# Kernel tuning notes

Hardware: AMD Instinct MI355X
Metric: run time of the kernel (lower is better)

Reference implementation:

```python
import jax, jax.numpy as jnp
import numpy as np
from jax import lax

DIM = 64
HEADS = 4
B, Q, V = 8, 128, 128


def _modrelu(z, b):
    m = jnp.abs(z)
    return z * (jax.nn.relu(m + b) / (m + 1e-5))


def _eunn_unitary(h, th1, ph1, th2, ph2, om):
    # tunable-style EUNN, capacity 2: even-pair rotations, odd-pair rotations, diagonal phase
    d = h.shape[-1]
    # layer 1: pairs (0,1),(2,3),...
    hp = h.reshape(*h.shape[:-1], d // 2, 2)
    a, b = hp[..., 0], hp[..., 1]
    c1, s1, e1 = jnp.cos(th1), jnp.sin(th1), jnp.exp(1j * ph1)
    h = jnp.stack([e1 * (c1 * a - s1 * b), s1 * a + c1 * b], -1).reshape(h.shape)
    # layer 2: pairs (1,2),(3,4),...,(d-3,d-2); endpoints pass through
    mid = h[..., 1:d - 1].reshape(*h.shape[:-1], d // 2 - 1, 2)
    a, b = mid[..., 0], mid[..., 1]
    c2, s2, e2 = jnp.cos(th2), jnp.sin(th2), jnp.exp(1j * ph2)
    mid2 = jnp.stack([e2 * (c2 * a - s2 * b), s2 * a + c2 * b], -1).reshape(*h.shape[:-1], d - 2)
    h = jnp.concatenate([h[..., :1], mid2, h[..., d - 1:]], -1)
    return h * jnp.exp(1j * om)


def _forward(queries, values, U_re, U_im, bias, theta1, phi1, theta2, phi2, omega, W_dense, b_dense):
    Bq, Qq, d = queries.shape
    Vv = values.shape[1]
    # quadratic (query, value) expansion -> [B*Q, V, 2d]
    dq = jnp.broadcast_to(queries[:, :, None, :], (Bq, Qq, Vv, d))
    dv = jnp.broadcast_to(values[:, None, :, :], (Bq, Qq, Vv, d))
    x = jnp.concatenate([dq, dv], -1).reshape(Bq * Qq, Vv, 2 * d)
    U = (U_re + 1j * U_im)  # [H, 2d, d] complex input kernel per head
    Ux = jnp.einsum('nvi,hij->hvnj', x.astype(jnp.complex64), U)  # [H, V, N, d]

    def run_head(Ux_h, t1, p1, t2, p2, om, bh):
        def step(h, u):
            h2 = _modrelu(_eunn_unitary(h, t1, p1, t2, p2, om) + u, bh)
            return h2, None
        h0 = jnp.zeros(Ux_h.shape[1:], dtype=jnp.complex64)  # [N, d]
        hT, _ = lax.scan(step, h0, Ux_h)
        return hT  # final state, as Keras RNN with return_sequences=False

    outs = jax.vmap(run_head)(Ux, theta1, phi1, theta2, phi2, omega, bias)  # [H, N, d]
    acc = jnp.real(outs).transpose(1, 0, 2).reshape(Bq * Qq, HEADS * d)
    y = acc @ W_dense + b_dense
    return y.reshape(Bq, Qq, d)


def setup_inputs() -> dict:
    key = jax.random.key(0)
    ks = jax.random.split(key, 12)
    pi = np.pi
    return {
        'queries': jax.random.normal(ks[0], (B, Q, DIM), jnp.float32),
        'values': jax.random.normal(ks[1], (B, V, DIM), jnp.float32),
        'U_re': jax.random.normal(ks[2], (HEADS, 2 * DIM, DIM), jnp.float32) * (1.0 / np.sqrt(2 * DIM)),
        'U_im': jax.random.normal(ks[3], (HEADS, 2 * DIM, DIM), jnp.float32) * (1.0 / np.sqrt(2 * DIM)),
        'bias': jax.random.normal(ks[4], (HEADS, DIM), jnp.float32) * 0.01,
        'theta1': jax.random.uniform(ks[5], (HEADS, DIM // 2), jnp.float32, -pi, pi),
        'phi1': jax.random.uniform(ks[6], (HEADS, DIM // 2), jnp.float32, -pi, pi),
        'theta2': jax.random.uniform(ks[7], (HEADS, DIM // 2 - 1), jnp.float32, -pi, pi),
        'phi2': jax.random.uniform(ks[8], (HEADS, DIM // 2 - 1), jnp.float32, -pi, pi),
        'omega': jax.random.uniform(ks[9], (HEADS, DIM), jnp.float32, -pi, pi),
        'W_dense': jax.random.normal(ks[10], (HEADS * DIM, DIM), jnp.float32) * (1.0 / np.sqrt(HEADS * DIM)),
        'b_dense': jnp.zeros((DIM,), jnp.float32),
    }


def reference(queries, values, U_re, U_im, bias, theta1, phi1, theta2, phi2, omega, W_dense, b_dense):
    return _forward(queries, values, U_re, U_im, bias, theta1, phi1, theta2, phi2, omega, W_dense, b_dense)
```

## Files before the change

### kernel.cpp

```cpp
#include <hip/hip_runtime.h>
#include <math.h>

#define DIM 64
#define HEADS 4
#define BB 8
#define QQ 128
#define VV 128
#define NN (BB*QQ)

typedef float f2 __attribute__((ext_vector_type(2)));

__device__ __forceinline__ float dpp_swap1(float x) {
    return __int_as_float(__builtin_amdgcn_update_dpp(
        0, __float_as_int(x), 0xB1, 0xF, 0xF, true));
}
__device__ __forceinline__ float dpp_wshr1(float x) {
    return __int_as_float(__builtin_amdgcn_update_dpp(
        0, __float_as_int(x), 0x138, 0xF, 0xF, true));
}
__device__ __forceinline__ float dpp_wshl1(float x) {
    return __int_as_float(__builtin_amdgcn_update_dpp(
        0, __float_as_int(x), 0x130, 0xF, 0xF, true));
}
__device__ __forceinline__ f2 dpp2_swap1(f2 x) {
    f2 r; r.x = dpp_swap1(x.x); r.y = dpp_swap1(x.y); return r;
}
__device__ __forceinline__ f2 dpp2_shl1(f2 x) {
    f2 r; r.x = dpp_wshl1(x.x); r.y = dpp_wshl1(x.y); return r;
}
__device__ __forceinline__ f2 dpp2_shr1(f2 x) {
    f2 r; r.x = dpp_wshr1(x.x); r.y = dpp_wshr1(x.y); return r;
}

__global__ __launch_bounds__(256) void k_av(const float* __restrict__ values,
                                            const float* __restrict__ U_re,
                                            const float* __restrict__ U_im,
                                            f2* __restrict__ Av) {
    int tid = blockIdx.x * blockDim.x + threadIdx.x;
    int w = tid >> 6;
    int j = tid & 63;
    int h = w >> 8;
    int r0 = (w & 255) << 2;
    const float* vrow = values + r0 * DIM;
    const float* ur = U_re + (h * 2 * DIM + DIM) * DIM + j;
    const float* ui = U_im + (h * 2 * DIM + DIM) * DIM + j;
    f2 a0 = 0.f, a1 = 0.f, a2 = 0.f, a3 = 0.f;
    #pragma unroll 8
    for (int i = 0; i < DIM; ++i) {
        f2 u; u.x = ur[i * DIM]; u.y = ui[i * DIM];
        a0 += vrow[i] * u;
        a1 += vrow[DIM + i] * u;
        a2 += vrow[2 * DIM + i] * u;
        a3 += vrow[3 * DIM + i] * u;
    }
    f2* out = Av + (h * 1024 + r0) * DIM + j;
    out[0] = a0; out[DIM] = a1; out[2 * DIM] = a2; out[3 * DIM] = a3;
}

__global__ __launch_bounds__(256) void k_rnn_dense(
        const float* __restrict__ queries,
        const float* __restrict__ U_re,
        const float* __restrict__ U_im,
        const float* __restrict__ bias,
        const float* __restrict__ theta1,
        const float* __restrict__ phi1,
        const float* __restrict__ theta2,
        const float* __restrict__ phi2,
        const float* __restrict__ omega,
        const f2* __restrict__ Av,
        const float* __restrict__ W_dense,
        const float* __restrict__ b_dense,
        float* __restrict__ y) {
    int b = blockIdx.x >> 6;
    int q = blockIdx.x & 63;
    int t = threadIdx.x;
    int h = t >> 6;
    int j = t & 63;
    int n0 = b * 128 + q;
    int n1 = n0 + 64;

    int k1 = j >> 1;
    float th1 = theta1[h * 32 + k1], ph1 = phi1[h * 32 + k1];
    float c1 = cosf(th1), s1 = sinf(th1);
    float A1r, A1i, B1r, B1i;
    if ((j & 1) == 0) {
        float er = cosf(ph1), ei = sinf(ph1);
        A1r = er * c1; A1i = ei * c1;
        B1r = -er * s1; B1i = -ei * s1;
    } else {
        A1r = c1; A1i = 0.f;
        B1r = s1; B1i = 0.f;
    }

    float A2r, A2i, BLr, BLi, BRr, BRi;
    if (j == 0 || j == 63) {
        A2r = 1.f; A2i = 0.f; BLr = 0.f; BLi = 0.f; BRr = 0.f; BRi = 0.f;
    } else {
        int k2 = (j - 1) >> 1;
        float th2 = theta2[h * 31 + k2], ph2 = phi2[h * 31 + k2];
        float c2 = cosf(th2), s2 = sinf(th2);
        if (j & 1) {
            float er = cosf(ph2), ei = sinf(ph2);
            A2r = er * c2; A2i = ei * c2;
            BLr = -er * s2; BLi = -ei * s2;
            BRr = 0.f; BRi = 0.f;
        } else {
            A2r = c2; A2i = 0.f;
            BRr = s2; BRi = 0.f;
            BLr = 0.f; BLi = 0.f;
        }
    }
    {
        float om = omega[h * 64 + j];
        float eor = cosf(om), eoi = sinf(om);
        float tr, ti;
        tr = A2r * eor - A2i * eoi; ti = A2r * eoi + A2i * eor; A2r = tr; A2i = ti;
        tr = BLr * eor - BLi * eoi; ti = BLr * eoi + BLi * eor; BLr = tr; BLi = ti;
        tr = BRr * eor - BRi * eoi; ti = BRr * eoi + BRi * eor; BRr = tr; BRi = ti;
    }
    float bj = bias[h * 64 + j];

    const float* qrow0 = queries + n0 * DIM;
    const float* qrow1 = queries + n1 * DIM;
    const float* ur = U_re + (h * 2 * DIM) * DIM + j;
    const float* ui = U_im + (h * 2 * DIM) * DIM + j;
    f2 Uqr = 0.f, Uqi = 0.f;
    #pragma unroll 8
    for (int i = 0; i < DIM; ++i) {
        f2 a; a.x = qrow0[i]; a.y = qrow1[i];
        float wr = ur[i * DIM], wi = ui[i * DIM];
        Uqr += a * wr;
        Uqi += a * wi;
    }

    const f2* Avp = Av + (h * 1024 + b * 128) * DIM + j;

    f2 Hr = 0.f, Hi = 0.f;
    f2 av = Avp[0];
    f2 uvr = Uqr + av.x, uvi = Uqi + av.y;
    #pragma unroll 4
    for (int v = 0; v < VV; ++v) {
        f2 avn = Avp[((v + 1) & 127) * DIM];
        f2 Pr = dpp2_swap1(Hr), Pi = dpp2_swap1(Hi);
        f2 Tr = (A1r * Hr - A1i * Hi) + (B1r * Pr - B1i * Pi);
        f2 Ti = (A1r * Hi + A1i * Hr) + (B1r * Pi + B1i * Pr);
        f2 Lr = dpp2_shl1(Tr), Li = dpp2_shl1(Ti);
        f2 Rr = dpp2_shr1(Tr), Ri = dpp2_shr1(Ti);
        f2 Sr = (A2r * Tr - A2i * Ti) + (BLr * Lr - BLi * Li) + (BRr * Rr - BRi * Ri);
        f2 Si = (A2r * Ti + A2i * Tr) + (BLr * Li + BLi * Lr) + (BRr * Ri + BRi * Rr);
        f2 Zr = Sr + uvr;
        f2 Zi = Si + uvi;
        uvr = Uqr + avn.x; uvi = Uqi + avn.y;
        f2 q2 = Zr * Zr + Zi * Zi + 1e-10f;
        f2 rs; rs.x = __builtin_amdgcn_rsqf(q2.x); rs.y = __builtin_amdgcn_rsqf(q2.y);
        f2 tp = q2 * rs + bj;
        tp.x = fmaxf(tp.x, 0.f); tp.y = fmaxf(tp.y, 0.f);
        f2 sc = tp * rs;
        Hr = Zr * sc; Hi = Zi * sc;
        av = avn;
    }

    __shared__ float s_acc[2][HEADS * DIM];
    __shared__ float s_part[256];
    s_acc[0][h * 64 + j] = Hr.x;
    s_acc[1][h * 64 + j] = Hr.y;
    __syncthreads();

    {
        int r = t >> 7, hf = (t >> 6) & 1, jj = t & 63;
        const float* Wp = W_dense + (hf * 128) * DIM + jj;
        const float* ap = &s_acc[r][hf * 128];
        float part = 0.f;
        #pragma unroll 8
        for (int k = 0; k < 128; ++k)
            part = fmaf(ap[k], Wp[k * DIM], part);
        s_part[t] = part;
    }
    __syncthreads();
    if (t < 128) {
        int r = t >> 6, jj = t & 63;
        y[(n0 + r * 64) * DIM + jj] =
            b_dense[jj] + s_part[r * 128 + jj] + s_part[r * 128 + 64 + jj];
    }
}

extern "C" void kernel_launch(void* const* d_in, const int* in_sizes, int n_in,
                              void* d_out, int out_size, void* d_ws, size_t ws_size,
                              hipStream_t stream) {
    const float* queries = (const float*)d_in[0];
    const float* values  = (const float*)d_in[1];
    const float* U_re    = (const float*)d_in[2];
    const float* U_im    = (const float*)d_in[3];
    const float* bias    = (const float*)d_in[4];
    const float* theta1  = (const float*)d_in[5];
    const float* phi1    = (const float*)d_in[6];
    const float* theta2  = (const float*)d_in[7];
    const float* phi2    = (const float*)d_in[8];
    const float* omega   = (const float*)d_in[9];
    const float* W_dense = (const float*)d_in[10];
    const float* b_dense = (const float*)d_in[11];
    float* y = (float*)d_out;

    f2* Av = (f2*)d_ws;

    k_av<<<256, 256, 0, stream>>>(values, U_re, U_im, Av);
    k_rnn_dense<<<512, 256, 0, stream>>>(queries, U_re, U_im, bias, theta1,
                                         phi1, theta2, phi2, omega, Av,
                                         W_dense, b_dense, y);
}
```

Baseline: 118.1 us.

## Process one sequence per block instead of two to double block count

```diff
diff --git a/kernel.cpp b/kernel.cpp
--- a/kernel.cpp
+++ b/kernel.cpp
@@ -21,15 +21,6 @@
 __device__ __forceinline__ float dpp_wshl1(float x) {
     return __int_as_float(__builtin_amdgcn_update_dpp(
         0, __float_as_int(x), 0x130, 0xF, 0xF, true));
-}
-__device__ __forceinline__ f2 dpp2_swap1(f2 x) {
-    f2 r; r.x = dpp_swap1(x.x); r.y = dpp_swap1(x.y); return r;
-}
-__device__ __forceinline__ f2 dpp2_shl1(f2 x) {
-    f2 r; r.x = dpp_wshl1(x.x); r.y = dpp_wshl1(x.y); return r;
-}
-__device__ __forceinline__ f2 dpp2_shr1(f2 x) {
-    f2 r; r.x = dpp_wshr1(x.x); r.y = dpp_wshr1(x.y); return r;
 }
 
 __global__ __launch_bounds__(256) void k_av(const float* __restrict__ values,
@@ -57,7 +48,7 @@
     out[0] = a0; out[DIM] = a1; out[2 * DIM] = a2; out[3 * DIM] = a3;
 }
 
-__global__ __launch_bounds__(256) void k_rnn_dense(
+__global__ __launch_bounds__(256, 4) void k_rnn_dense(
         const float* __restrict__ queries,
         const float* __restrict__ U_re,
         const float* __restrict__ U_im,
@@ -71,13 +62,11 @@
         const float* __restrict__ W_dense,
         const float* __restrict__ b_dense,
         float* __restrict__ y) {
-    int b = blockIdx.x >> 6;
-    int q = blockIdx.x & 63;
+    int n = blockIdx.x;
     int t = threadIdx.x;
     int h = t >> 6;
     int j = t & 63;
-    int n0 = b * 128 + q;
-    int n1 = n0 + 64;
+    int b = n >> 7;
 
     int k1 = j >> 1;
     float th1 = theta1[h * 32 + k1], ph1 = phi1[h * 32 + k1];
@@ -120,67 +109,63 @@
     }
     float bj = bias[h * 64 + j];
 
-    const float* qrow0 = queries + n0 * DIM;
-    const float* qrow1 = queries + n1 * DIM;
+    const float* qrow = queries + n * DIM;
     const float* ur = U_re + (h * 2 * DIM) * DIM + j;
     const float* ui = U_im + (h * 2 * DIM) * DIM + j;
-    f2 Uqr = 0.f, Uqi = 0.f;
+    float uqr = 0.f, uqi = 0.f;
     #pragma unroll 8
     for (int i = 0; i < DIM; ++i) {
-        f2 a; a.x = qrow0[i]; a.y = qrow1[i];
-        float wr = ur[i * DIM], wi = ui[i * DIM];
-        Uqr += a * wr;
-        Uqi += a * wi;
+        float a = qrow[i];
+        uqr = fmaf(a, ur[i * DIM], uqr);
+        uqi = fmaf(a, ui[i * DIM], uqi);
     }
 
     const f2* Avp = Av + (h * 1024 + b * 128) * DIM + j;
 
-    f2 Hr = 0.f, Hi = 0.f;
-    f2 av = Avp[0];
-    f2 uvr = Uqr + av.x, uvi = Uqi + av.y;
+    float hr = 0.f, hi = 0.f;
+    f2 av0 = Avp[0];
+    float uvr = uqr + av0.x, uvi = uqi + av0.y;
+    f2 avn = Avp[DIM];
     #pragma unroll 4
     for (int v = 0; v < VV; ++v) {
-        f2 avn = Avp[((v + 1) & 127) * DIM];
-        f2 Pr = dpp2_swap1(Hr), Pi = dpp2_swap1(Hi);
-        f2 Tr = (A1r * Hr - A1i * Hi) + (B1r * Pr - B1i * Pi);
-        f2 Ti = (A1r * Hi + A1i * Hr) + (B1r * Pi + B1i * Pr);
-        f2 Lr = dpp2_shl1(Tr), Li = dpp2_shl1(Ti);
-        f2 Rr = dpp2_shr1(Tr), Ri = dpp2_shr1(Ti);
-        f2 Sr = (A2r * Tr - A2i * Ti) + (BLr * Lr - BLi * Li) + (BRr * Rr - BRi * Ri);
-        f2 Si = (A2r * Ti + A2i * Tr) + (BLr * Li + BLi * Lr) + (BRr * Ri + BRi * Rr);
-        f2 Zr = Sr + uvr;
-        f2 Zi = Si + uvi;
-        uvr = Uqr + avn.x; uvi = Uqi + avn.y;
-        f2 q2 = Zr * Zr + Zi * Zi + 1e-10f;
-        f2 rs; rs.x = __builtin_amdgcn_rsqf(q2.x); rs.y = __builtin_amdgcn_rsqf(q2.y);
-        f2 tp = q2 * rs + bj;
-        tp.x = fmaxf(tp.x, 0.f); tp.y = fmaxf(tp.y, 0.f);
-        f2 sc = tp * rs;
-        Hr = Zr * sc; Hi = Zi * sc;
-        av = avn;
+        f2 av2 = Avp[((v + 2) & 127) * DIM];
+        float pr = dpp_swap1(hr), pi = dpp_swap1(hi);
+        float t_r = (A1r * hr - A1i * hi) + (B1r * pr - B1i * pi);
+        float t_i = (A1r * hi + A1i * hr) + (B1r * pi + B1i * pr);
+        float Lr = dpp_wshl1(t_r), Li = dpp_wshl1(t_i);
+        float Rr = dpp_wshr1(t_r), Ri = dpp_wshr1(t_i);
+        float s_r = (A2r * t_r - A2i * t_i) + (BLr * Lr - BLi * Li) + (BRr * Rr - BRi * Ri);
+        float s_i = (A2r * t_i + A2i * t_r) + (BLr * Li + BLi * Lr) + (BRr * Ri + BRi * Rr);
+        float zr = s_r + uvr;
+        float zi = s_i + uvi;
+        uvr = uqr + avn.x; uvi = uqi + avn.y;
+        avn = av2;
+        float q2 = fmaf(zr, zr, fmaf(zi, zi, 1e-10f));
+        float rs = __builtin_amdgcn_rsqf(q2);
+        float tp = fmaxf(fmaf(q2, rs, bj), 0.f);
+        float sc = tp * rs;
+        hr = zr * sc; hi = zi * sc;
     }
 
-    __shared__ float s_acc[2][HEADS * DIM];
+    __shared__ float s_acc[HEADS * DIM];
     __shared__ float s_part[256];
-    s_acc[0][h * 64 + j] = Hr.x;
-    s_acc[1][h * 64 + j] = Hr.y;
+    s_acc[h * 64 + j] = hr;
     __syncthreads();
 
     {
-        int r = t >> 7, hf = (t >> 6) & 1, jj = t & 63;
-        const float* Wp = W_dense + (hf * 128) * DIM + jj;
-        const float* ap = &s_acc[r][hf * 128];
+        int qq = t >> 6, jj = t & 63;
+        const float* Wp = W_dense + (qq * 64) * DIM + jj;
+        const float* ap = &s_acc[qq * 64];
         float part = 0.f;
         #pragma unroll 8
-        for (int k = 0; k < 128; ++k)
+        for (int k = 0; k < 64; ++k)
             part = fmaf(ap[k], Wp[k * DIM], part);
         s_part[t] = part;
     }
     __syncthreads();
-    if (t < 128) {
-        int r = t >> 6, jj = t & 63;
-        y[(n0 + r * 64) * DIM + jj] =
-            b_dense[jj] + s_part[r * 128 + jj] + s_part[r * 128 + 64 + jj];
+    if (t < 64) {
+        y[n * DIM + t] = b_dense[t] + s_part[t] + s_part[64 + t]
+                       + s_part[128 + t] + s_part[192 + t];
     }
 }
 
@@ -204,7 +189,7 @@
     f2* Av = (f2*)d_ws;
 
     k_av<<<256, 256, 0, stream>>>(values, U_re, U_im, Av);
-    k_rnn_dense<<<512, 256, 0, stream>>>(queries, U_re, U_im, bias, theta1,
-                                         phi1, theta2, phi2, omega, Av,
-                                         W_dense, b_dense, y);
+    k_rnn_dense<<<1024, 256, 0, stream>>>(queries, U_re, U_im, bias, theta1,
+                                          phi1, theta2, phi2, omega, Av,
+                                          W_dense, b_dense, y);
 }
```

Measured after the change: 131.5 us. 11.3% more time.
